# Kernel optimization log

Hardware: AMD Instinct MI355X
Metric: run time of the kernel (lower is better)

## Reference

```python
import jax, jax.numpy as jnp
import numpy as np

N = 200000
E = 3200000


def _init_linear(key, fan_in, fan_out):
    kw, kb = jax.random.split(key)
    bound = 1.0 / np.sqrt(fan_in)
    W = jax.random.uniform(kw, (fan_in, fan_out), jnp.float32, -bound, bound)
    b = jax.random.uniform(kb, (fan_out,), jnp.float32, -bound, bound)
    return W, b


def setup_inputs() -> dict:
    key = jax.random.key(0)
    ks = jax.random.split(key, 8)
    latent_features = jax.random.normal(ks[0], (N, 256), jnp.float32)
    history = jax.random.uniform(ks[1], (N,), jnp.float32)
    is_subgoal = jax.random.uniform(ks[2], (N,), jnp.float32)
    edge_index = jax.random.randint(ks[3], (2, E), 0, N, dtype=jnp.int64)
    W1, b1 = _init_linear(ks[4], 258, 128)
    W2, b2 = _init_linear(ks[5], 128, 64)
    W3, b3 = _init_linear(ks[6], 64, 8)
    Wc, bc = _init_linear(ks[7], 8, 3)
    return {"latent_features": latent_features, "history": history,
            "is_subgoal": is_subgoal, "edge_index": edge_index,
            "W1": W1, "b1": b1, "W2": W2, "b2": b2,
            "W3": W3, "b3": b3, "Wc": Wc, "bc": bc}


def _gcn_conv(h, W, b, src, dst, norm, n):
    # PyG GCNConv: linear transform, then symmetric-normalized scatter-add.
    h = h @ W                                  # [n, F_out]
    msg = norm[:, None] * h[src]               # gather + edge-norm, [E+n, F_out]
    out = jax.ops.segment_sum(msg, dst, num_segments=n)
    return out + b


def reference(latent_features, history, is_subgoal, edge_index,
              W1, b1, W2, b2, W3, b3, Wc, bc):
    n = latent_features.shape[0]
    # add self-loops (GCNConv default add_self_loops=True)
    loop = jnp.arange(n, dtype=edge_index.dtype)
    src = jnp.concatenate([edge_index[0], loop])
    dst = jnp.concatenate([edge_index[1], loop])
    # symmetric normalization: deg over destination (incl. self-loops)
    deg = jax.ops.segment_sum(jnp.ones_like(dst, dtype=jnp.float32), dst,
                              num_segments=n)
    dinv = jnp.where(deg > 0, jax.lax.rsqrt(deg), 0.0)
    norm = dinv[src] * dinv[dst]               # [E+n]

    h = jnp.concatenate([latent_features, history[:, None],
                         is_subgoal[:, None]], axis=1)  # [n, 258]
    h = jax.nn.relu(_gcn_conv(h, W1, b1, src, dst, norm, n))
    h = jax.nn.relu(_gcn_conv(h, W2, b2, src, dst, norm, n))
    h = jax.nn.relu(_gcn_conv(h, W3, b3, src, dst, norm, n))
    return h @ Wc + bc                          # [n, 3]
```

## Files before the change

kernel.cpp:

```cpp
#include <hip/hip_runtime.h>
#include <hip/hip_fp16.h>


#define N_NODES 200000
#define N_EDGES 3200000
#define NBUCK 782

static_assert(N_NODES % 64 == 0, "tiling");
static_assert((NBUCK - 1) * 256 < N_NODES && NBUCK * 256 >= N_NODES, "buckets");

typedef unsigned int u32;


__global__ __launch_bounds__(256) void k_bhist(const int* __restrict__ dst,
                                               int* __restrict__ bcnt) {
    __shared__ int lh[NBUCK];
    int t = threadIdx.x;
    for (int b = t; b < NBUCK; b += 256) lh[b] = 0;
    __syncthreads();
    long e0 = (long)blockIdx.x * 8192;
    for (int k = 0; k < 32; ++k) {
        long e = e0 + k * 256 + t;
        if (e < N_EDGES) atomicAdd(&lh[dst[e] >> 8], 1);
    }
    __syncthreads();
    for (int b = t; b < NBUCK; b += 256)
        if (lh[b]) atomicAdd(&bcnt[b], lh[b]);
}


__global__ __launch_bounds__(256) void k_bscan(const int* __restrict__ bcnt,
                                               int* __restrict__ boff,
                                               int* __restrict__ bcur,
                                               int* __restrict__ row) {
    __shared__ int sm[256];
    int t = threadIdx.x;
    int base = t * 4;
    int a0 = (base + 0 < NBUCK) ? bcnt[base + 0] : 0;
    int a1 = (base + 1 < NBUCK) ? bcnt[base + 1] : 0;
    int a2 = (base + 2 < NBUCK) ? bcnt[base + 2] : 0;
    int a3 = (base + 3 < NBUCK) ? bcnt[base + 3] : 0;
    int s = a0 + a1 + a2 + a3;
    sm[t] = s;
    __syncthreads();
    for (int o = 1; o < 256; o <<= 1) {
        int v = (t >= o) ? sm[t - o] : 0;
        __syncthreads();
        sm[t] += v;
        __syncthreads();
    }
    int excl = sm[t] - s;
    if (base + 0 < NBUCK) { boff[base + 0] = excl;               bcur[base + 0] = excl; }
    if (base + 1 < NBUCK) { boff[base + 1] = excl + a0;          bcur[base + 1] = excl + a0; }
    if (base + 2 < NBUCK) { boff[base + 2] = excl + a0 + a1;     bcur[base + 2] = excl + a0 + a1; }
    if (base + 3 < NBUCK) { boff[base + 3] = excl + a0 + a1 + a2; bcur[base + 3] = excl + a0 + a1 + a2; }
    if (t == 255) { boff[NBUCK] = N_EDGES; row[N_NODES] = N_EDGES; }
}


__global__ __launch_bounds__(256) void k_scatter(const int* __restrict__ src,
                                                 const int* __restrict__ dst,
                                                 int* __restrict__ bcur,
                                                 u32* __restrict__ entries) {
    __shared__ int lh[NBUCK];
    __shared__ int base[NBUCK];
    __shared__ int lcur[NBUCK];
    int t = threadIdx.x;
    for (int b = t; b < NBUCK; b += 256) lh[b] = 0;
    __syncthreads();
    long e0 = (long)blockIdx.x * 8192;
    for (int k = 0; k < 32; ++k) {
        long e = e0 + k * 256 + t;
        if (e < N_EDGES) atomicAdd(&lh[dst[e] >> 8], 1);
    }
    __syncthreads();
    for (int b = t; b < NBUCK; b += 256) {
        base[b] = atomicAdd(&bcur[b], lh[b]);
        lcur[b] = 0;
    }
    __syncthreads();
    for (int k = 0; k < 32; ++k) {
        long e = e0 + k * 256 + t;
        if (e < N_EDGES) {
            int d = dst[e];
            int bkt = d >> 8;
            int p = base[bkt] + atomicAdd(&lcur[bkt], 1);
            entries[p] = ((u32)src[e] << 8) | (u32)(d & 255);
        }
    }
}


__global__ __launch_bounds__(256) void k_prep(const u32* __restrict__ entries,
                                              const int* __restrict__ boff,
                                              int* __restrict__ row,
                                              float* __restrict__ dinv,
                                              int* __restrict__ col) {
    __shared__ int lh[256];
    __shared__ int sc[256];
    __shared__ int cur[256];
    const int b = blockIdx.x, t = threadIdx.x;
    const int s = boff[b], e = boff[b + 1];
    const int cnt = e - s;
    lh[t] = 0;
    __syncthreads();
    for (int i = t; i < cnt; i += 256) atomicAdd(&lh[entries[s + i] & 255], 1);
    __syncthreads();
    int my = lh[t];
    sc[t] = my;
    __syncthreads();
    for (int o = 1; o < 256; o <<= 1) {
        int v = (t >= o) ? sc[t - o] : 0;
        __syncthreads();
        sc[t] += v;
        __syncthreads();
    }
    int excl = sc[t] - my;
    int node = b * 256 + t;
    if (node < N_NODES) {
        row[node] = s + excl;
        dinv[node] = rsqrtf((float)(my + 1));
    }
    cur[t] = s + excl;
    __syncthreads();
    for (int i = t; i < cnt; i += 256) {
        u32 en = entries[s + i];
        int p = atomicAdd(&cur[en & 255], 1);
        col[p] = (int)(en >> 8);
    }
}


__global__ __launch_bounds__(256) void k_gemm1(const float* __restrict__ X,
                                               const float* __restrict__ hist,
                                               const float* __restrict__ subg,
                                               const float* __restrict__ W,
                                               const float* __restrict__ dinv,
                                               __half2* __restrict__ g1) {
    __shared__ float Xs[128][33];
    __shared__ float Ws[32][132];
    const int t = threadIdx.x;
    const int nb = blockIdx.x * 128;
    const int fi = t & 15;
    const int ni = t >> 4;
    const int lxn = t >> 1;
    const int lxk = (t & 1) * 16;
    const int lwk = t >> 3;
    const int lwf = (t & 7) * 16;

    float acc[8][8];
#pragma unroll
    for (int n = 0; n < 8; ++n)
#pragma unroll
        for (int f = 0; f < 8; ++f) acc[n][f] = 0.f;

    int xrow = nb + lxn;
    if (xrow >= N_NODES) xrow = N_NODES - 1;

    for (int kc = 0; kc < 256; kc += 32) {
        const float* xp = X + (size_t)xrow * 256 + kc + lxk;
        float4* xsp = (float4*)&Xs[lxn][lxk];
        xsp[0] = *(const float4*)(xp + 0);
        xsp[1] = *(const float4*)(xp + 4);
        xsp[2] = *(const float4*)(xp + 8);
        xsp[3] = *(const float4*)(xp + 12);

        const float* wp = W + (size_t)(kc + lwk) * 128 + lwf;
        float4* wsp = (float4*)&Ws[lwk][lwf];
        wsp[0] = *(const float4*)(wp + 0);
        wsp[1] = *(const float4*)(wp + 4);
        wsp[2] = *(const float4*)(wp + 8);
        wsp[3] = *(const float4*)(wp + 12);
        __syncthreads();

#pragma unroll
        for (int kk = 0; kk < 32; ++kk) {
            float4 wa = *(const float4*)&Ws[kk][fi * 4];
            float4 wb = *(const float4*)&Ws[kk][64 + fi * 4];
#pragma unroll
            for (int n = 0; n < 8; ++n) {
                float xv = Xs[ni * 8 + n][kk];
                acc[n][0] += xv * wa.x;
                acc[n][1] += xv * wa.y;
                acc[n][2] += xv * wa.z;
                acc[n][3] += xv * wa.w;
                acc[n][4] += xv * wb.x;
                acc[n][5] += xv * wb.y;
                acc[n][6] += xv * wb.z;
                acc[n][7] += xv * wb.w;
            }
        }
        __syncthreads();
    }

    float w256[8], w257[8];
#pragma unroll
    for (int f = 0; f < 4; ++f) {
        w256[f] = W[256 * 128 + fi * 4 + f];
        w257[f] = W[257 * 128 + fi * 4 + f];
        w256[4 + f] = W[256 * 128 + 64 + fi * 4 + f];
        w257[4 + f] = W[257 * 128 + 64 + fi * 4 + f];
    }
#pragma unroll
    for (int n = 0; n < 8; ++n) {
        int node = nb + ni * 8 + n;
        if (node >= N_NODES) break;
        float hh = hist[node];
        float ss = subg[node];
        float dv = dinv[node];
        float2 pa, pb;
        __half2* ha = (__half2*)&pa;
        __half2* hb = (__half2*)&pb;
#pragma unroll
        for (int k = 0; k < 2; ++k) {
            __half2 va, vb;
            va.x = __float2half_rn((acc[n][2 * k + 0] + hh * w256[2 * k + 0] + ss * w257[2 * k + 0]) * dv);
            va.y = __float2half_rn((acc[n][2 * k + 1] + hh * w256[2 * k + 1] + ss * w257[2 * k + 1]) * dv);
            vb.x = __float2half_rn((acc[n][4 + 2 * k + 0] + hh * w256[4 + 2 * k + 0] + ss * w257[4 + 2 * k + 0]) * dv);
            vb.y = __float2half_rn((acc[n][4 + 2 * k + 1] + hh * w256[4 + 2 * k + 1] + ss * w257[4 + 2 * k + 1]) * dv);
            ha[k] = va;
            hb[k] = vb;
        }
        *(float2*)(g1 + (size_t)node * 64 + fi * 2) = pa;
        *(float2*)(g1 + (size_t)node * 64 + 32 + fi * 2) = pb;
    }
}


__global__ __launch_bounds__(256) void k_gemm2(const float* __restrict__ Xin,
                                               const float* __restrict__ W,
                                               const float* __restrict__ dinv,
                                               __half2* __restrict__ g2) {
    __shared__ float Xs[64][33];
    __shared__ float Ws[32][68];
    const int t = threadIdx.x;
    const int nb = blockIdx.x * 64;
    const int fi = t & 15;
    const int ni = t >> 4;
    const int lxn = t >> 2;
    const int lxk = (t & 3) * 8;
    const int lwk = t >> 3;
    const int lwf = (t & 7) * 8;

    float acc[4][4];
#pragma unroll
    for (int n = 0; n < 4; ++n)
#pragma unroll
        for (int f = 0; f < 4; ++f) acc[n][f] = 0.f;

    for (int kc = 0; kc < 128; kc += 32) {
        const float* xp = Xin + (size_t)(nb + lxn) * 128 + kc + lxk;
        float4 xa = *(const float4*)xp;
        float4 xb = *(const float4*)(xp + 4);
        Xs[lxn][lxk + 0] = xa.x;
        Xs[lxn][lxk + 1] = xa.y;
        Xs[lxn][lxk + 2] = xa.z;
        Xs[lxn][lxk + 3] = xa.w;
        Xs[lxn][lxk + 4] = xb.x;
        Xs[lxn][lxk + 5] = xb.y;
        Xs[lxn][lxk + 6] = xb.z;
        Xs[lxn][lxk + 7] = xb.w;

        const float* wp = W + (size_t)(kc + lwk) * 64 + lwf;
        float4* wsp = (float4*)&Ws[lwk][lwf];
        wsp[0] = *(const float4*)(wp + 0);
        wsp[1] = *(const float4*)(wp + 4);
        __syncthreads();

#pragma unroll
        for (int kk = 0; kk < 32; ++kk) {
            float4 wv = *(const float4*)&Ws[kk][fi * 4];
#pragma unroll
            for (int n = 0; n < 4; ++n) {
                float xv = Xs[ni * 4 + n][kk];
                acc[n][0] += xv * wv.x;
                acc[n][1] += xv * wv.y;
                acc[n][2] += xv * wv.z;
                acc[n][3] += xv * wv.w;
            }
        }
        __syncthreads();
    }

#pragma unroll
    for (int n = 0; n < 4; ++n) {
        float dv = dinv[nb + ni * 4 + n];
        float2 pk;
        __half2* ph = (__half2*)&pk;
#pragma unroll
        for (int k = 0; k < 2; ++k) {
            __half2 h;
            h.x = __float2half_rn(acc[n][2 * k + 0] * dv);
            h.y = __float2half_rn(acc[n][2 * k + 1] * dv);
            ph[k] = h;
        }
        *(float2*)(g2 + (size_t)(nb + ni * 4 + n) * 32 + fi * 2) = pk;
    }
}


__global__ __launch_bounds__(256) void k_gemm3(const float* __restrict__ Xin,
                                               const float* __restrict__ W,
                                               const float* __restrict__ dinv,
                                               float* __restrict__ g3) {
    __shared__ float Ws[512];
    int t = threadIdx.x;
    Ws[t] = W[t];
    Ws[t + 256] = W[t + 256];
    __syncthreads();
    int i = blockIdx.x * 256 + t;
    if (i >= N_NODES) return;
    const float4* xp = (const float4*)(Xin + (size_t)i * 64);
    float acc[8];
#pragma unroll
    for (int f = 0; f < 8; ++f) acc[f] = 0.f;
#pragma unroll
    for (int k4 = 0; k4 < 16; ++k4) {
        float4 xv = xp[k4];
        float xs[4] = {xv.x, xv.y, xv.z, xv.w};
#pragma unroll
        for (int q = 0; q < 4; ++q) {
            int k = k4 * 4 + q;
            float4 w0 = *(const float4*)&Ws[k * 8];
            float4 w1 = *(const float4*)&Ws[k * 8 + 4];
            acc[0] += xs[q] * w0.x;
            acc[1] += xs[q] * w0.y;
            acc[2] += xs[q] * w0.z;
            acc[3] += xs[q] * w0.w;
            acc[4] += xs[q] * w1.x;
            acc[5] += xs[q] * w1.y;
            acc[6] += xs[q] * w1.z;
            acc[7] += xs[q] * w1.w;
        }
    }
    float dv = dinv[i];
    float* op = g3 + (size_t)i * 8;
    *(float4*)op = make_float4(acc[0] * dv, acc[1] * dv, acc[2] * dv, acc[3] * dv);
    *(float4*)(op + 4) = make_float4(acc[4] * dv, acc[5] * dv, acc[6] * dv, acc[7] * dv);
}


template <int F, int TPN>
__global__ __launch_bounds__(256) void k_aggh(const __half2* __restrict__ g,
                                              const int* __restrict__ row,
                                              const int* __restrict__ col,
                                              const float* __restrict__ dinv,
                                              const float* __restrict__ bias,
                                              float* __restrict__ out) {
    constexpr int H2 = F / 2;
    static_assert(TPN == H2, "one half2 per lane");
    constexpr int NPB = 256 / TPN;
    const int t = threadIdx.x;
    const int node = blockIdx.x * NPB + t / TPN;
    const int lane = t % TPN;

    float ax = 0.f, ay = 0.f;
    const int s = row[node];
    const int e = row[node + 1];
    int idx = s;
    for (; idx + 8 <= e; idx += 8) {
        int j[8];
#pragma unroll
        for (int u = 0; u < 8; ++u) j[u] = col[idx + u];
        __half2 h[8];
#pragma unroll
        for (int u = 0; u < 8; ++u) h[u] = g[(size_t)j[u] * H2 + lane];
#pragma unroll
        for (int u = 0; u < 8; ++u) {
            float2 f = __half22float2(h[u]);
            ax += f.x;
            ay += f.y;
        }
    }
    for (; idx < e; ++idx) {
        float2 f = __half22float2(g[(size_t)col[idx] * H2 + lane]);
        ax += f.x;
        ay += f.y;
    }
    float2 fs = __half22float2(g[(size_t)node * H2 + lane]);
    const float di = dinv[node];
    float2 b = *(const float2*)(bias + lane * 2);
    float2 o;
    o.x = fmaxf(di * (ax + fs.x) + b.x, 0.f);
    o.y = fmaxf(di * (ay + fs.y) + b.y, 0.f);
    *(float2*)(out + (size_t)node * F + lane * 2) = o;
}


__global__ __launch_bounds__(256) void k_agg8(const float* __restrict__ g,
                                              const int* __restrict__ row,
                                              const int* __restrict__ col,
                                              const float* __restrict__ dinv,
                                              const float* __restrict__ bias,
                                              float* __restrict__ out) {
    const int t = threadIdx.x;
    const int node = blockIdx.x * 32 + t / 8;
    const int lane = t & 7;
    float acc = 0.f;
    const int s = row[node];
    const int e = row[node + 1];
    int idx = s;
    for (; idx + 8 <= e; idx += 8) {
        int j[8];
#pragma unroll
        for (int u = 0; u < 8; ++u) j[u] = col[idx + u];
        float v[8];
#pragma unroll
        for (int u = 0; u < 8; ++u) v[u] = g[(size_t)j[u] * 8 + lane];
#pragma unroll
        for (int u = 0; u < 8; ++u) acc += v[u];
    }
    for (; idx < e; ++idx) acc += g[(size_t)col[idx] * 8 + lane];
    acc += g[(size_t)node * 8 + lane];
    out[(size_t)node * 8 + lane] = fmaxf(dinv[node] * acc + bias[lane], 0.f);
}


__global__ __launch_bounds__(256) void k_final(const float* __restrict__ h,
                                               const float* __restrict__ Wc,
                                               const float* __restrict__ bc,
                                               float* __restrict__ out) {
    int i = blockIdx.x * 256 + threadIdx.x;
    if (i >= N_NODES) return;
    const float4* xp = (const float4*)(h + (size_t)i * 8);
    float4 x0 = xp[0], x1 = xp[1];
    float xs[8] = {x0.x, x0.y, x0.z, x0.w, x1.x, x1.y, x1.z, x1.w};
    float o0 = bc[0], o1 = bc[1], o2 = bc[2];
#pragma unroll
    for (int k = 0; k < 8; ++k) {
        o0 += xs[k] * Wc[k * 3 + 0];
        o1 += xs[k] * Wc[k * 3 + 1];
        o2 += xs[k] * Wc[k * 3 + 2];
    }
    out[(size_t)i * 3 + 0] = o0;
    out[(size_t)i * 3 + 1] = o1;
    out[(size_t)i * 3 + 2] = o2;
}


extern "C" void kernel_launch(void* const* d_in, const int* in_sizes, int n_in,
                              void* d_out, int out_size, void* d_ws, size_t ws_size,
                              hipStream_t stream) {
    const float* latent = (const float*)d_in[0];
    const float* hist = (const float*)d_in[1];
    const float* subg = (const float*)d_in[2];
    const int* eidx = (const int*)d_in[3];
    const float* W1 = (const float*)d_in[4];
    const float* b1 = (const float*)d_in[5];
    const float* W2 = (const float*)d_in[6];
    const float* b2 = (const float*)d_in[7];
    const float* W3 = (const float*)d_in[8];
    const float* b3 = (const float*)d_in[9];
    const float* Wc = (const float*)d_in[10];
    const float* bc = (const float*)d_in[11];
    float* outp = (float*)d_out;

    char* ws = (char*)d_ws;
    size_t off = 0;
    auto take = [&](size_t bytes) -> void* {
        void* p = ws + off;
        off += (bytes + 255) & ~(size_t)255;
        return p;
    };
    float* dinv = (float*)take((size_t)N_NODES * 4);
    int* row = (int*)take((size_t)(N_NODES + 1) * 4);
    int* col = (int*)take((size_t)N_EDGES * 4);
    u32* entries = (u32*)take((size_t)N_EDGES * 4);
    int* bcnt = (int*)take((size_t)NBUCK * 4);
    int* boff = (int*)take((size_t)(NBUCK + 1) * 4);
    int* bcur = (int*)take((size_t)NBUCK * 4);
    __half2* bufH = (__half2*)take((size_t)N_NODES * 128 * 2);
    float* bufA = (float*)take((size_t)N_NODES * 128 * 4);
    float* bufB = (float*)take((size_t)N_NODES * 64 * 4);

    const int* srcp = eidx;
    const int* dstp = eidx + N_EDGES;

    const int scat_blocks = (N_EDGES + 8191) / 8192;

    hipMemsetAsync(bcnt, 0, (size_t)NBUCK * 4, stream);
    k_bhist<<<scat_blocks, 256, 0, stream>>>(dstp, bcnt);
    k_bscan<<<1, 256, 0, stream>>>(bcnt, boff, bcur, row);
    k_scatter<<<scat_blocks, 256, 0, stream>>>(srcp, dstp, bcur, entries);
    k_prep<<<NBUCK, 256, 0, stream>>>(entries, boff, row, dinv, col);

    k_gemm1<<<(N_NODES + 127) / 128, 256, 0, stream>>>(latent, hist, subg, W1, dinv, bufH);
    k_aggh<128, 64><<<N_NODES / 4, 256, 0, stream>>>(bufH, row, col, dinv, b1, bufA);
    k_gemm2<<<N_NODES / 64, 256, 0, stream>>>(bufA, W2, dinv, bufH);
    k_aggh<64, 32><<<N_NODES / 8, 256, 0, stream>>>(bufH, row, col, dinv, b2, bufB);
    k_gemm3<<<(N_NODES + 255) / 256, 256, 0, stream>>>(bufB, W3, dinv, bufA);
    k_agg8<<<N_NODES / 32, 256, 0, stream>>>(bufA, row, col, dinv, b3, bufB);
    k_final<<<(N_NODES + 255) / 256, 256, 0, stream>>>(bufB, Wc, bc, outp);
}
```

Baseline: 867.8 us.

## Run first-layer GEMM on MFMA using split fp16 hi/lo operands

Replaces the fp32 FMA register-tiled first-layer GEMM with MFMA 16x16x32 f16 instructions. Both X and W are split into high and low fp16 parts, and three products are summed to keep close to fp32 accuracy. A new small kernel pre-transposes and splits W1 into fp16 halves, and X loads for the next k-chunk are register-prefetched. The aim is to cut the compute cost of the largest GEMM, at the price of three MFMA passes, W fragments read directly from global memory, and some precision risk.

```diff
diff --git a/kernel.cpp b/kernel.cpp
--- a/kernel.cpp
+++ b/kernel.cpp
@@ -10,6 +10,9 @@
 static_assert((NBUCK - 1) * 256 < N_NODES && NBUCK * 256 >= N_NODES, "buckets");
 
 typedef unsigned int u32;
+typedef _Float16 f16;
+typedef __attribute__((ext_vector_type(8))) _Float16 f16x8;
+typedef __attribute__((ext_vector_type(4))) float f32x4;
 
 
 __global__ __launch_bounds__(256) void k_bhist(const int* __restrict__ dst,
@@ -131,98 +134,127 @@
 }
 
 
+__global__ __launch_bounds__(256) void k_prepw(const float* __restrict__ W,
+                                               f16* __restrict__ Wth,
+                                               f16* __restrict__ Wtl) {
+    int t = blockIdx.x * 256 + threadIdx.x;
+    int k = t >> 7;
+    int f = t & 127;
+    float w = W[k * 128 + f];
+    f16 hi = (f16)w;
+    f16 lo = (f16)(w - (float)hi);
+    Wth[f * 256 + k] = hi;
+    Wtl[f * 256 + k] = lo;
+}
+
+
 __global__ __launch_bounds__(256) void k_gemm1(const float* __restrict__ X,
                                                const float* __restrict__ hist,
                                                const float* __restrict__ subg,
                                                const float* __restrict__ W,
+                                               const f16* __restrict__ Wth,
+                                               const f16* __restrict__ Wtl,
                                                const float* __restrict__ dinv,
                                                __half2* __restrict__ g1) {
-    __shared__ float Xs[128][33];
-    __shared__ float Ws[32][132];
+    __shared__ f16 Ah[128][40];
+    __shared__ f16 Al[128][40];
     const int t = threadIdx.x;
     const int nb = blockIdx.x * 128;
-    const int fi = t & 15;
-    const int ni = t >> 4;
-    const int lxn = t >> 1;
-    const int lxk = (t & 1) * 16;
-    const int lwk = t >> 3;
-    const int lwf = (t & 7) * 16;
-
-    float acc[8][8];
-#pragma unroll
-    for (int n = 0; n < 8; ++n)
-#pragma unroll
-        for (int f = 0; f < 8; ++f) acc[n][f] = 0.f;
-
-    int xrow = nb + lxn;
+    const int wv = t >> 6;
+    const int l = t & 63;
+    const int l15 = l & 15;
+    const int lk = l >> 4;
+
+    const int srow = t >> 1;
+    const int skh = (t & 1) * 16;
+    int xrow = nb + srow;
     if (xrow >= N_NODES) xrow = N_NODES - 1;
+    const float* xbase = X + (size_t)xrow * 256 + skh;
+
+    f32x4 acc[8][2];
+#pragma unroll
+    for (int fb = 0; fb < 8; ++fb)
+#pragma unroll
+        for (int nf = 0; nf < 2; ++nf) acc[fb][nf] = (f32x4){0.f, 0.f, 0.f, 0.f};
+
+    float4 pre0 = *(const float4*)(xbase + 0);
+    float4 pre1 = *(const float4*)(xbase + 4);
+    float4 pre2 = *(const float4*)(xbase + 8);
+    float4 pre3 = *(const float4*)(xbase + 12);
+
+    const int nloc0 = wv * 32 + l15;
 
     for (int kc = 0; kc < 256; kc += 32) {
-        const float* xp = X + (size_t)xrow * 256 + kc + lxk;
-        float4* xsp = (float4*)&Xs[lxn][lxk];
-        xsp[0] = *(const float4*)(xp + 0);
-        xsp[1] = *(const float4*)(xp + 4);
-        xsp[2] = *(const float4*)(xp + 8);
-        xsp[3] = *(const float4*)(xp + 12);
-
-        const float* wp = W + (size_t)(kc + lwk) * 128 + lwf;
-        float4* wsp = (float4*)&Ws[lwk][lwf];
-        wsp[0] = *(const float4*)(wp + 0);
-        wsp[1] = *(const float4*)(wp + 4);
-        wsp[2] = *(const float4*)(wp + 8);
-        wsp[3] = *(const float4*)(wp + 12);
-        __syncthreads();
-
-#pragma unroll
-        for (int kk = 0; kk < 32; ++kk) {
-            float4 wa = *(const float4*)&Ws[kk][fi * 4];
-            float4 wb = *(const float4*)&Ws[kk][64 + fi * 4];
-#pragma unroll
-            for (int n = 0; n < 8; ++n) {
-                float xv = Xs[ni * 8 + n][kk];
-                acc[n][0] += xv * wa.x;
-                acc[n][1] += xv * wa.y;
-                acc[n][2] += xv * wa.z;
-                acc[n][3] += xv * wa.w;
-                acc[n][4] += xv * wb.x;
-                acc[n][5] += xv * wb.y;
-                acc[n][6] += xv * wb.z;
-                acc[n][7] += xv * wb.w;
+        if (kc) __syncthreads();
+
+        {
+            float xs[16] = {pre0.x, pre0.y, pre0.z, pre0.w,
+                            pre1.x, pre1.y, pre1.z, pre1.w,
+                            pre2.x, pre2.y, pre2.z, pre2.w,
+                            pre3.x, pre3.y, pre3.z, pre3.w};
+            union { f16 h[16]; f16x8 v[2]; } H, L;
+#pragma unroll
+            for (int i = 0; i < 16; ++i) {
+                f16 h = (f16)xs[i];
+                H.h[i] = h;
+                L.h[i] = (f16)(xs[i] - (float)h);
             }
-        }
-        __syncthreads();
-    }
-
-    float w256[8], w257[8];
-#pragma unroll
-    for (int f = 0; f < 4; ++f) {
-        w256[f] = W[256 * 128 + fi * 4 + f];
-        w257[f] = W[257 * 128 + fi * 4 + f];
-        w256[4 + f] = W[256 * 128 + 64 + fi * 4 + f];
-        w257[4 + f] = W[257 * 128 + 64 + fi * 4 + f];
-    }
-#pragma unroll
-    for (int n = 0; n < 8; ++n) {
-        int node = nb + ni * 8 + n;
-        if (node >= N_NODES) break;
-        float hh = hist[node];
-        float ss = subg[node];
-        float dv = dinv[node];
-        float2 pa, pb;
-        __half2* ha = (__half2*)&pa;
-        __half2* hb = (__half2*)&pb;
-#pragma unroll
-        for (int k = 0; k < 2; ++k) {
-            __half2 va, vb;
-            va.x = __float2half_rn((acc[n][2 * k + 0] + hh * w256[2 * k + 0] + ss * w257[2 * k + 0]) * dv);
-            va.y = __float2half_rn((acc[n][2 * k + 1] + hh * w256[2 * k + 1] + ss * w257[2 * k + 1]) * dv);
-            vb.x = __float2half_rn((acc[n][4 + 2 * k + 0] + hh * w256[4 + 2 * k + 0] + ss * w257[4 + 2 * k + 0]) * dv);
-            vb.y = __float2half_rn((acc[n][4 + 2 * k + 1] + hh * w256[4 + 2 * k + 1] + ss * w257[4 + 2 * k + 1]) * dv);
-            ha[k] = va;
-            hb[k] = vb;
-        }
-        *(float2*)(g1 + (size_t)node * 64 + fi * 2) = pa;
-        *(float2*)(g1 + (size_t)node * 64 + 32 + fi * 2) = pb;
+            *(f16x8*)&Ah[srow][skh + 0] = H.v[0];
+            *(f16x8*)&Ah[srow][skh + 8] = H.v[1];
+            *(f16x8*)&Al[srow][skh + 0] = L.v[0];
+            *(f16x8*)&Al[srow][skh + 8] = L.v[1];
+        }
+
+        if (kc + 32 < 256) {
+            const float* xp = xbase + kc + 32;
+            pre0 = *(const float4*)(xp + 0);
+            pre1 = *(const float4*)(xp + 4);
+            pre2 = *(const float4*)(xp + 8);
+            pre3 = *(const float4*)(xp + 12);
+        }
+        __syncthreads();
+
+        f16x8 xh0 = *(const f16x8*)&Ah[nloc0][lk * 8];
+        f16x8 xl0 = *(const f16x8*)&Al[nloc0][lk * 8];
+        f16x8 xh1 = *(const f16x8*)&Ah[nloc0 + 16][lk * 8];
+        f16x8 xl1 = *(const f16x8*)&Al[nloc0 + 16][lk * 8];
+
+        const f16* wbh = Wth + (size_t)l15 * 256 + kc + lk * 8;
+        const f16* wbl = Wtl + (size_t)l15 * 256 + kc + lk * 8;
+#pragma unroll
+        for (int fb = 0; fb < 8; ++fb) {
+            f16x8 wh = *(const f16x8*)(wbh + (size_t)fb * 16 * 256);
+            f16x8 wl = *(const f16x8*)(wbl + (size_t)fb * 16 * 256);
+            acc[fb][0] = __builtin_amdgcn_mfma_f32_16x16x32_f16(wh, xh0, acc[fb][0], 0, 0, 0);
+            acc[fb][0] = __builtin_amdgcn_mfma_f32_16x16x32_f16(wh, xl0, acc[fb][0], 0, 0, 0);
+            acc[fb][0] = __builtin_amdgcn_mfma_f32_16x16x32_f16(wl, xh0, acc[fb][0], 0, 0, 0);
+            acc[fb][1] = __builtin_amdgcn_mfma_f32_16x16x32_f16(wh, xh1, acc[fb][1], 0, 0, 0);
+            acc[fb][1] = __builtin_amdgcn_mfma_f32_16x16x32_f16(wh, xl1, acc[fb][1], 0, 0, 0);
+            acc[fb][1] = __builtin_amdgcn_mfma_f32_16x16x32_f16(wl, xh1, acc[fb][1], 0, 0, 0);
+        }
+    }
+
+#pragma unroll
+    for (int nf = 0; nf < 2; ++nf) {
+        int node = nb + wv * 32 + nf * 16 + l15;
+        bool ok = node < N_NODES;
+        int nc = ok ? node : (N_NODES - 1);
+        float hh = hist[nc];
+        float ss = subg[nc];
+        float dv = dinv[nc];
+        char* orow = (char*)g1 + (size_t)node * 256;
+#pragma unroll
+        for (int fb = 0; fb < 8; ++fb) {
+            int f0 = fb * 16 + lk * 4;
+            float4 w6 = *(const float4*)(W + 256 * 128 + f0);
+            float4 w7 = *(const float4*)(W + 257 * 128 + f0);
+            union { f16 h[4]; float2 v; } o;
+            o.h[0] = (f16)((acc[fb][nf][0] + hh * w6.x + ss * w7.x) * dv);
+            o.h[1] = (f16)((acc[fb][nf][1] + hh * w6.y + ss * w7.y) * dv);
+            o.h[2] = (f16)((acc[fb][nf][2] + hh * w6.z + ss * w7.z) * dv);
+            o.h[3] = (f16)((acc[fb][nf][3] + hh * w6.w + ss * w7.w) * dv);
+            if (ok) *(float2*)(orow + fb * 32 + lk * 8) = o.v;
+        }
     }
 }
 
@@ -472,6 +504,8 @@
     __half2* bufH = (__half2*)take((size_t)N_NODES * 128 * 2);
     float* bufA = (float*)take((size_t)N_NODES * 128 * 4);
     float* bufB = (float*)take((size_t)N_NODES * 64 * 4);
+    f16* Wth = (f16*)take((size_t)128 * 256 * 2);
+    f16* Wtl = (f16*)take((size_t)128 * 256 * 2);
 
     const int* srcp = eidx;
     const int* dstp = eidx + N_EDGES;
@@ -479,12 +513,13 @@
     const int scat_blocks = (N_EDGES + 8191) / 8192;
 
     hipMemsetAsync(bcnt, 0, (size_t)NBUCK * 4, stream);
+    k_prepw<<<128, 256, 0, stream>>>(W1, Wth, Wtl);
     k_bhist<<<scat_blocks, 256, 0, stream>>>(dstp, bcnt);
     k_bscan<<<1, 256, 0, stream>>>(bcnt, boff, bcur, row);
     k_scatter<<<scat_blocks, 256, 0, stream>>>(srcp, dstp, bcur, entries);
     k_prep<<<NBUCK, 256, 0, stream>>>(entries, boff, row, dinv, col);
 
-    k_gemm1<<<(N_NODES + 127) / 128, 256, 0, stream>>>(latent, hist, subg, W1, dinv, bufH);
+    k_gemm1<<<(N_NODES + 127) / 128, 256, 0, stream>>>(latent, hist, subg, W1, Wth, Wtl, dinv, bufH);
     k_aggh<128, 64><<<N_NODES / 4, 256, 0, stream>>>(bufH, row, col, dinv, b1, bufA);
     k_gemm2<<<N_NODES / 64, 256, 0, stream>>>(bufA, W2, dinv, bufH);
     k_aggh<64, 32><<<N_NODES / 8, 256, 0, stream>>>(bufH, row, col, dinv, b2, bufB);
```

Measured after the change: 891.3 us. +2.7%, slower.
